# Optimization experiments

Hardware: AMD Instinct MI355X
Metric: run time of the kernel (lower is better)

The kernel has to match this reference:

```python
import jax, jax.numpy as jnp
import numpy as np

B, N, D = 4, 2048, 1024
H = 16
DH = D // H  # 64
SCALE = DH ** -0.5


def setup_inputs() -> dict:
    key = jax.random.key(0)
    k1, k2, k3 = jax.random.split(key, 3)
    x = jax.random.normal(k1, (B, N, D), dtype=jnp.float32)
    W_qkv = jax.random.normal(k2, (D, 3 * D), dtype=jnp.float32) / np.sqrt(D)
    b_qkv = jnp.zeros((3 * D,), dtype=jnp.float32)
    W_out = jax.random.normal(k3, (D, D), dtype=jnp.float32) / np.sqrt(D)
    b_out = jnp.zeros((D,), dtype=jnp.float32)
    return {"x": x, "W_qkv": W_qkv, "b_qkv": b_qkv, "W_out": W_out, "b_out": b_out}


def reference(x, W_qkv, b_qkv, W_out, b_out):
    b, n, f = x.shape
    # fused QKV projection: [b, n, 3*D] -> [3, b, H, n, DH]
    qkv = (x @ W_qkv + b_qkv).reshape(b, n, 3, H, DH).transpose(2, 0, 3, 1, 4)
    q, k, v = qkv[0], qkv[1], qkv[2]
    # scaled dot-product attention (dropout rate is 0.0 -> identity)
    attn = jnp.einsum("bhqd,bhkd->bhqk", q, k) * SCALE
    attn = jax.nn.softmax(attn, axis=-1)
    out = jnp.einsum("bhqk,bhkd->bhqd", attn, v)  # [b, H, n, DH]
    out = out.transpose(0, 2, 1, 3).reshape(b, n, f)
    return out @ W_out + b_out
```

## Files before the change

### kernel.cpp

```cpp
#include <hip/hip_runtime.h>
#include <hip/hip_bf16.h>

typedef __bf16 bf16x8 __attribute__((ext_vector_type(8)));
typedef float f32x4 __attribute__((ext_vector_type(4)));
typedef unsigned short u16x8 __attribute__((ext_vector_type(8)));
typedef unsigned int u32x4 __attribute__((ext_vector_type(4)));

__device__ inline unsigned short f2bf(float f) {
  __hip_bfloat16 h = __float2bfloat16(f);
  return __builtin_bit_cast(unsigned short, h);
}

__device__ inline f32x4 zero4() {
  f32x4 z;
  #pragma unroll
  for (int i = 0; i < 4; ++i) z[i] = 0.0f;
  return z;
}

__device__ inline unsigned int pkbf(float lo, float hi) {
  unsigned int a = __builtin_bit_cast(unsigned int, lo) + 0x8000u;
  unsigned int b = __builtin_bit_cast(unsigned int, hi) + 0x8000u;
  return __builtin_amdgcn_perm(b, a, 0x07060302u);
}

__device__ inline void gload16(const unsigned short* g, unsigned short* l) {
  __builtin_amdgcn_global_load_lds(
      (const __attribute__((address_space(1))) unsigned int*)g,
      (__attribute__((address_space(3))) unsigned int*)l, 16, 0, 0);
}

#define QSCALE 0.18033688011112042f

__global__ __launch_bounds__(256) void cast_x_kernel(const float* __restrict__ in,
                                                     unsigned short* __restrict__ out, int n4) {
  int i = blockIdx.x * 256 + threadIdx.x;
  if (i < n4) {
    float4 v = ((const float4*)in)[i];
    ushort4 o;
    o.x = f2bf(v.x); o.y = f2bf(v.y); o.z = f2bf(v.z); o.w = f2bf(v.w);
    ((ushort4*)out)[i] = o;
  }
}

__global__ __launch_bounds__(256) void transpose_cast_kernel(const float* __restrict__ in,
                                                             unsigned short* __restrict__ out,
                                                             int R, int C) {
  __shared__ float tile[32][33];
  int c0 = blockIdx.x * 32, r0 = blockIdx.y * 32;
  int tx = threadIdx.x, ty = threadIdx.y;
  #pragma unroll
  for (int i = 0; i < 4; i++)
    tile[ty + i * 8][tx] = in[(size_t)(r0 + ty + i * 8) * C + c0 + tx];
  __syncthreads();
  #pragma unroll
  for (int i = 0; i < 4; i++)
    out[(size_t)(c0 + ty + i * 8) * R + r0 + tx] = f2bf(tile[tx][ty + i * 8]);
}

__global__ __launch_bounds__(256) void transpose_v_kernel(const unsigned short* __restrict__ V,
                                                          unsigned short* __restrict__ Vst) {
  __shared__ unsigned short tl[32][33];
  int k0 = blockIdx.x * 32, d0 = blockIdx.y * 32, bh = blockIdx.z;
  int tx = threadIdx.x, ty = threadIdx.y;
  #pragma unroll
  for (int i = 0; i < 4; i++)
    tl[ty + i * 8][tx] = V[((size_t)bh * 2048 + k0 + ty + i * 8) * 64 + d0 + tx];
  __syncthreads();
  #pragma unroll
  for (int i = 0; i < 4; i++) {
    int dd = d0 + ty + i * 8;
    int tok = k0 + tx;
    int tile = tok >> 6, k = tok & 63;
    Vst[((size_t)bh * 32 + tile) * 4096 + dd * 64 + (((k >> 3) ^ (dd & 7)) * 8) + (k & 7)] =
        tl[tx][ty + i * 8];
  }
}

template <int KDIM>
__device__ inline void gemm_tile(const unsigned short* __restrict__ A,
                                 const unsigned short* __restrict__ BT,
                                 int m0, int n0,
                                 unsigned short* ldsA, unsigned short* ldsB,
                                 f32x4 acc[4][4]) {
  const int t = threadIdx.x;
  const int lane = t & 63;
  const int w = t >> 6;
  const int wm = w >> 1, wn = w & 1;
  const int fr = lane & 15;
  const int fg = lane >> 4;
  const int srow = w * 8 + (lane >> 3);
  const int scol = (lane & 7) * 8;

  #pragma unroll
  for (int m = 0; m < 4; m++)
    #pragma unroll
    for (int n = 0; n < 4; n++) acc[m][n] = zero4();

  for (int kt = 0; kt < KDIM / 64; ++kt) {
    __syncthreads();
    #pragma unroll
    for (int i = 0; i < 4; i++) {
      int row = i * 32 + srow;
      gload16(A + (size_t)(m0 + row) * KDIM + kt * 64 + scol, ldsA + row * 64 + scol);
      gload16(BT + (size_t)(n0 + row) * KDIM + kt * 64 + scol, ldsB + row * 64 + scol);
    }
    __syncthreads();
    #pragma unroll
    for (int ks = 0; ks < 2; ++ks) {
      bf16x8 a[4], b[4];
      #pragma unroll
      for (int m = 0; m < 4; m++)
        a[m] = *(const bf16x8*)(ldsA + (wm * 64 + m * 16 + fr) * 64 + ks * 32 + fg * 8);
      #pragma unroll
      for (int n = 0; n < 4; n++)
        b[n] = *(const bf16x8*)(ldsB + (wn * 64 + n * 16 + fr) * 64 + ks * 32 + fg * 8);
      #pragma unroll
      for (int m = 0; m < 4; m++)
        #pragma unroll
        for (int n = 0; n < 4; n++)
          acc[m][n] = __builtin_amdgcn_mfma_f32_16x16x32_bf16(a[m], b[n], acc[m][n], 0, 0, 0);
    }
  }
}

__global__ __launch_bounds__(256) void gemm_qkv_kernel(const unsigned short* __restrict__ xbf,
                                                       const unsigned short* __restrict__ WqkvT,
                                                       const float* __restrict__ bqkv,
                                                       unsigned short* __restrict__ Qws,
                                                       unsigned short* __restrict__ Kst,
                                                       unsigned short* __restrict__ Vws) {
  __shared__ unsigned short ldsA[128 * 64];
  __shared__ unsigned short ldsB[128 * 64];
  int m0 = blockIdx.y * 128, n0 = blockIdx.x * 128;
  f32x4 acc[4][4];
  gemm_tile<1024>(xbf, WqkvT, m0, n0, ldsA, ldsB, acc);

  const int lane = threadIdx.x & 63;
  const int w = threadIdx.x >> 6;
  const int wm = w >> 1, wn = w & 1;
  const int fr = lane & 15, fg = lane >> 4;
  #pragma unroll
  for (int m = 0; m < 4; m++) {
    #pragma unroll
    for (int n = 0; n < 4; n++) {
      int col = n0 + wn * 64 + n * 16 + fr;
      int s = col >> 10, cc = col & 1023, h = cc >> 6, d = cc & 63;
      float bias = bqkv[col];
      #pragma unroll
      for (int r = 0; r < 4; r++) {
        int row = m0 + wm * 64 + m * 16 + fg * 4 + r;
        int bb = row >> 11, tok = row & 2047;
        int bh = bb * 16 + h;
        float val = acc[m][n][r] + bias;
        if (s == 0) {
          Qws[((size_t)bh * 2048 + tok) * 64 + d] = f2bf(val * QSCALE);
        } else if (s == 1) {
          int kk = tok & 63, tile = tok >> 6;
          int w32 = kk & 31;
          int sg = ((kk >> 5) * 2 + ((w32 >> 2) & 1)) * 16 + ((w32 >> 3) << 2) + (w32 & 3);
          Kst[((size_t)bh * 32 + tile) * 4096 + sg * 64 + (((d >> 3) ^ (sg & 7)) * 8) + (d & 7)] =
              f2bf(val);
        } else {
          Vws[((size_t)bh * 2048 + tok) * 64 + d] = f2bf(val);
        }
      }
    }
  }
}

__global__ __launch_bounds__(256) void attn_kernel(const unsigned short* __restrict__ Qws,
                                                   const unsigned short* __restrict__ Kst,
                                                   const unsigned short* __restrict__ Vst,
                                                   unsigned short* __restrict__ attn_out) {
  __shared__ unsigned short ldsK[2][4096];
  __shared__ unsigned short ldsV[2][4096];
  const int t = threadIdx.x, lane = t & 63, w = t >> 6;
  int bid = blockIdx.x;
  int vid = (bid & 7) * 128 + (bid >> 3);
  const int bh = vid >> 4, qt = vid & 15;
  const int q0 = qt * 128;
  const int fr = lane & 15, fg = lane >> 4, sw = fr & 7;
  const size_t bhbase = (size_t)bh * 2048;

  bf16x8 qf[2][2];
  #pragma unroll
  for (int u = 0; u < 2; u++) {
    const unsigned short* qrow = Qws + (bhbase + q0 + w * 32 + u * 16 + fr) * 64;
    qf[u][0] = *(const bf16x8*)(qrow + fg * 8);
    qf[u][1] = *(const bf16x8*)(qrow + 32 + fg * 8);
  }

  f32x4 lvec[2];
  f32x4 ot[2][4];
  #pragma unroll
  for (int u = 0; u < 2; u++) {
    lvec[u] = zero4();
    #pragma unroll
    for (int dt = 0; dt < 4; dt++) ot[u][dt] = zero4();
  }

  const unsigned short* kbase = Kst + (size_t)bh * 32 * 4096 + w * 1024 + lane * 8;
  const unsigned short* vbase = Vst + (size_t)bh * 32 * 4096 + w * 1024 + lane * 8;
  unsigned short* kl0 = &ldsK[0][0] + w * 1024 + lane * 8;
  unsigned short* vl0 = &ldsV[0][0] + w * 1024 + lane * 8;

  gload16(kbase, kl0);           gload16(kbase + 512, kl0 + 512);
  gload16(vbase, vl0);           gload16(vbase + 512, vl0 + 512);

  for (int tt2 = 0; tt2 < 32; tt2 += 2) {
    #pragma unroll
    for (int half = 0; half < 2; half++) {
      const int tt = tt2 + half;
      __syncthreads();
      if (tt + 1 < 32) {
        const unsigned short* kg = kbase + (size_t)(tt + 1) * 4096;
        const unsigned short* vg = vbase + (size_t)(tt + 1) * 4096;
        unsigned short* kd = (half ? kl0 : kl0 + 4096);
        unsigned short* vd = (half ? vl0 : vl0 + 4096);
        gload16(kg, kd);            gload16(kg + 512, kd + 512);
        gload16(vg, vd);            gload16(vg + 512, vd + 512);
      }
      const unsigned short* Kb = &ldsK[half][0];
      const unsigned short* Vb = &ldsV[half][0];

      f32x4 st[2][4];
      __builtin_amdgcn_s_setprio(1);
      #pragma unroll
      for (int c = 0; c < 4; c++) {
        const unsigned short* krow = Kb + (c * 16 + fr) * 64;
        bf16x8 a0 = *(const bf16x8*)(krow + ((fg ^ sw) * 8));
        bf16x8 a1 = *(const bf16x8*)(krow + (((4 + fg) ^ sw) * 8));
        #pragma unroll
        for (int u = 0; u < 2; u++) {
          st[u][c] = __builtin_amdgcn_mfma_f32_16x16x32_bf16(a0, qf[u][0], zero4(), 0, 0, 0);
          st[u][c] = __builtin_amdgcn_mfma_f32_16x16x32_bf16(a1, qf[u][1], st[u][c], 0, 0, 0);
        }
      }
      __builtin_amdgcn_s_setprio(0);

      u32x4 pb[2][2];
      #pragma unroll
      for (int u = 0; u < 2; u++) {
        #pragma unroll
        for (int c = 0; c < 4; c++) {
          #pragma unroll
          for (int r = 0; r < 4; r++) st[u][c][r] = exp2f(st[u][c][r]);
          lvec[u] += st[u][c];
        }
        #pragma unroll
        for (int kc = 0; kc < 2; kc++) {
          u32x4 pv;
          pv[0] = pkbf(st[u][kc * 2][0], st[u][kc * 2][1]);
          pv[1] = pkbf(st[u][kc * 2][2], st[u][kc * 2][3]);
          pv[2] = pkbf(st[u][kc * 2 + 1][0], st[u][kc * 2 + 1][1]);
          pv[3] = pkbf(st[u][kc * 2 + 1][2], st[u][kc * 2 + 1][3]);
          pb[u][kc] = pv;
        }
      }

      __builtin_amdgcn_s_setprio(1);
      #pragma unroll
      for (int dt = 0; dt < 4; dt++) {
        const unsigned short* vrow = Vb + (dt * 16 + fr) * 64;
        #pragma unroll
        for (int kc = 0; kc < 2; kc++) {
          bf16x8 av = *(const bf16x8*)(vrow + (((kc * 4 + fg) ^ sw) * 8));
          #pragma unroll
          for (int u = 0; u < 2; u++)
            ot[u][dt] = __builtin_amdgcn_mfma_f32_16x16x32_bf16(
                av, __builtin_bit_cast(bf16x8, pb[u][kc]), ot[u][dt], 0, 0, 0);
        }
      }
      __builtin_amdgcn_s_setprio(0);
    }
  }

  const int b = bh >> 4, h = bh & 15;
  #pragma unroll
  for (int u = 0; u < 2; u++) {
    float l = lvec[u][0] + lvec[u][1] + lvec[u][2] + lvec[u][3];
    l += __shfl_xor(l, 16, 64);
    l += __shfl_xor(l, 32, 64);
    float rl = 1.0f / l;
    int q = q0 + w * 32 + u * 16 + fr;
    #pragma unroll
    for (int dt = 0; dt < 4; dt++) {
      ushort4 o;
      o.x = f2bf(ot[u][dt][0] * rl);
      o.y = f2bf(ot[u][dt][1] * rl);
      o.z = f2bf(ot[u][dt][2] * rl);
      o.w = f2bf(ot[u][dt][3] * rl);
      int d = dt * 16 + fg * 4;
      *(ushort4*)(attn_out + ((size_t)b * 2048 + q) * 1024 + h * 64 + d) = o;
    }
  }
}

__global__ __launch_bounds__(256) void gemm_out_kernel(const unsigned short* __restrict__ attn,
                                                       const unsigned short* __restrict__ WoutT,
                                                       const float* __restrict__ bout,
                                                       float* __restrict__ out) {
  __shared__ unsigned short ldsA[128 * 64];
  __shared__ unsigned short ldsB[128 * 64];
  int m0 = blockIdx.y * 128, n0 = blockIdx.x * 128;
  f32x4 acc[4][4];
  gemm_tile<1024>(attn, WoutT, m0, n0, ldsA, ldsB, acc);

  const int lane = threadIdx.x & 63;
  const int w = threadIdx.x >> 6;
  const int wm = w >> 1, wn = w & 1;
  const int fr = lane & 15, fg = lane >> 4;
  #pragma unroll
  for (int m = 0; m < 4; m++) {
    #pragma unroll
    for (int n = 0; n < 4; n++) {
      int col = n0 + wn * 64 + n * 16 + fr;
      float bias = bout[col];
      #pragma unroll
      for (int r = 0; r < 4; r++) {
        int row = m0 + wm * 64 + m * 16 + fg * 4 + r;
        out[(size_t)row * 1024 + col] = acc[m][n][r] + bias;
      }
    }
  }
}

extern "C" void kernel_launch(void* const* d_in, const int* in_sizes, int n_in,
                              void* d_out, int out_size, void* d_ws, size_t ws_size,
                              hipStream_t stream) {
  const float* x = (const float*)d_in[0];
  const float* Wqkv = (const float*)d_in[1];
  const float* bqkv = (const float*)d_in[2];
  const float* Wout = (const float*)d_in[3];
  const float* bout = (const float*)d_in[4];
  float* out = (float*)d_out;

  unsigned short* xbf = (unsigned short*)d_ws;
  unsigned short* wqkvT = xbf + 8388608;
  unsigned short* woutT = wqkvT + 3145728;
  unsigned short* Qws = woutT + 1048576;
  unsigned short* Kst = Qws + 8388608;
  unsigned short* Vws = Kst + 8388608;
  unsigned short* Vst = Vws + 8388608;
  unsigned short* attn = xbf;

  cast_x_kernel<<<8192, 256, 0, stream>>>(x, xbf, 2097152);
  transpose_cast_kernel<<<dim3(96, 32), dim3(32, 8), 0, stream>>>(Wqkv, wqkvT, 1024, 3072);
  transpose_cast_kernel<<<dim3(32, 32), dim3(32, 8), 0, stream>>>(Wout, woutT, 1024, 1024);
  gemm_qkv_kernel<<<dim3(24, 64), 256, 0, stream>>>(xbf, wqkvT, bqkv, Qws, Kst, Vws);
  transpose_v_kernel<<<dim3(64, 2, 64), dim3(32, 8), 0, stream>>>(Vws, Vst);
  attn_kernel<<<1024, 256, 0, stream>>>(Qws, Kst, Vst, attn);
  gemm_out_kernel<<<dim3(8, 64), 256, 0, stream>>>(attn, woutT, bout, out);
}
```

Baseline: 345.1 us.

## Fuse V transpose into QKV GEMM epilogue and use native exp/bf16-pack instructions

The QKV GEMM epilogue now writes V directly in the swizzled transposed tile layout the attention kernel reads. This removes the separate transpose_v kernel launch and its extra round trip of V through global memory. The attention softmax also swaps exp2f for the raw v_exp_f32 instruction and a manual bf16 packing routine for v_cvt_pk_bf16_f32. The scattered 2-byte V stores in the epilogue are less coalesced, and the exp and bf16 rounding behaviour may differ slightly.

```diff
diff --git a/kernel.cpp b/kernel.cpp
--- a/kernel.cpp
+++ b/kernel.cpp
@@ -18,10 +18,16 @@
   return z;
 }
 
-__device__ inline unsigned int pkbf(float lo, float hi) {
-  unsigned int a = __builtin_bit_cast(unsigned int, lo) + 0x8000u;
-  unsigned int b = __builtin_bit_cast(unsigned int, hi) + 0x8000u;
-  return __builtin_amdgcn_perm(b, a, 0x07060302u);
+__device__ inline float exp2_fast(float x) {
+  float r;
+  asm("v_exp_f32 %0, %1" : "=v"(r) : "v"(x));
+  return r;
+}
+
+__device__ inline unsigned int cvtpk(float lo, float hi) {
+  unsigned int r;
+  asm("v_cvt_pk_bf16_f32 %0, %1, %2" : "=v"(r) : "v"(lo), "v"(hi));
+  return r;
 }
 
 __device__ inline void gload16(const unsigned short* g, unsigned short* l) {
@@ -56,25 +62,6 @@
   #pragma unroll
   for (int i = 0; i < 4; i++)
     out[(size_t)(c0 + ty + i * 8) * R + r0 + tx] = f2bf(tile[tx][ty + i * 8]);
-}
-
-__global__ __launch_bounds__(256) void transpose_v_kernel(const unsigned short* __restrict__ V,
-                                                          unsigned short* __restrict__ Vst) {
-  __shared__ unsigned short tl[32][33];
-  int k0 = blockIdx.x * 32, d0 = blockIdx.y * 32, bh = blockIdx.z;
-  int tx = threadIdx.x, ty = threadIdx.y;
-  #pragma unroll
-  for (int i = 0; i < 4; i++)
-    tl[ty + i * 8][tx] = V[((size_t)bh * 2048 + k0 + ty + i * 8) * 64 + d0 + tx];
-  __syncthreads();
-  #pragma unroll
-  for (int i = 0; i < 4; i++) {
-    int dd = d0 + ty + i * 8;
-    int tok = k0 + tx;
-    int tile = tok >> 6, k = tok & 63;
-    Vst[((size_t)bh * 32 + tile) * 4096 + dd * 64 + (((k >> 3) ^ (dd & 7)) * 8) + (k & 7)] =
-        tl[tx][ty + i * 8];
-  }
 }
 
 template <int KDIM>
@@ -129,7 +116,7 @@
                                                        const float* __restrict__ bqkv,
                                                        unsigned short* __restrict__ Qws,
                                                        unsigned short* __restrict__ Kst,
-                                                       unsigned short* __restrict__ Vws) {
+                                                       unsigned short* __restrict__ Vst) {
   __shared__ unsigned short ldsA[128 * 64];
   __shared__ unsigned short ldsB[128 * 64];
   int m0 = blockIdx.y * 128, n0 = blockIdx.x * 128;
@@ -162,7 +149,9 @@
           Kst[((size_t)bh * 32 + tile) * 4096 + sg * 64 + (((d >> 3) ^ (sg & 7)) * 8) + (d & 7)] =
               f2bf(val);
         } else {
-          Vws[((size_t)bh * 2048 + tok) * 64 + d] = f2bf(val);
+          int kk = tok & 63, tile = tok >> 6;
+          Vst[((size_t)bh * 32 + tile) * 4096 + d * 64 + (((kk >> 3) ^ (d & 7)) * 8) + (kk & 7)] =
+              f2bf(val);
         }
       }
     }
@@ -245,16 +234,16 @@
         #pragma unroll
         for (int c = 0; c < 4; c++) {
           #pragma unroll
-          for (int r = 0; r < 4; r++) st[u][c][r] = exp2f(st[u][c][r]);
+          for (int r = 0; r < 4; r++) st[u][c][r] = exp2_fast(st[u][c][r]);
           lvec[u] += st[u][c];
         }
         #pragma unroll
         for (int kc = 0; kc < 2; kc++) {
           u32x4 pv;
-          pv[0] = pkbf(st[u][kc * 2][0], st[u][kc * 2][1]);
-          pv[1] = pkbf(st[u][kc * 2][2], st[u][kc * 2][3]);
-          pv[2] = pkbf(st[u][kc * 2 + 1][0], st[u][kc * 2 + 1][1]);
-          pv[3] = pkbf(st[u][kc * 2 + 1][2], st[u][kc * 2 + 1][3]);
+          pv[0] = cvtpk(st[u][kc * 2][0], st[u][kc * 2][1]);
+          pv[1] = cvtpk(st[u][kc * 2][2], st[u][kc * 2][3]);
+          pv[2] = cvtpk(st[u][kc * 2 + 1][0], st[u][kc * 2 + 1][1]);
+          pv[3] = cvtpk(st[u][kc * 2 + 1][2], st[u][kc * 2 + 1][3]);
           pb[u][kc] = pv;
         }
       }
@@ -341,15 +330,13 @@
   unsigned short* woutT = wqkvT + 3145728;
   unsigned short* Qws = woutT + 1048576;
   unsigned short* Kst = Qws + 8388608;
-  unsigned short* Vws = Kst + 8388608;
-  unsigned short* Vst = Vws + 8388608;
+  unsigned short* Vst = Kst + 8388608;
   unsigned short* attn = xbf;
 
   cast_x_kernel<<<8192, 256, 0, stream>>>(x, xbf, 2097152);
   transpose_cast_kernel<<<dim3(96, 32), dim3(32, 8), 0, stream>>>(Wqkv, wqkvT, 1024, 3072);
   transpose_cast_kernel<<<dim3(32, 32), dim3(32, 8), 0, stream>>>(Wout, woutT, 1024, 1024);
-  gemm_qkv_kernel<<<dim3(24, 64), 256, 0, stream>>>(xbf, wqkvT, bqkv, Qws, Kst, Vws);
-  transpose_v_kernel<<<dim3(64, 2, 64), dim3(32, 8), 0, stream>>>(Vws, Vst);
+  gemm_qkv_kernel<<<dim3(24, 64), 256, 0, stream>>>(xbf, wqkvT, bqkv, Qws, Kst, Vst);
   attn_kernel<<<1024, 256, 0, stream>>>(Qws, Kst, Vst, attn);
   gemm_out_kernel<<<dim3(8, 64), 256, 0, stream>>>(attn, woutT, bout, out);
 }
```

Measured after the change: 301.9 us. -12.5%, faster.
